# Kernel tuning notes

Measured on AMD Instinct MI355X. Metric: run time of the kernel, lower is better.

The kernel has to match this reference:

```python
import jax, jax.numpy as jnp
import numpy as np

D_MODEL = 768
N_HEADS = 12
N_KV = 4
D_HEAD = 64
WINDOW = 512
GLOBAL = 64
THETA = 10000.0


def setup_inputs() -> dict:
    key = jax.random.key(0)
    ks = jax.random.split(key, 5)
    B, T = 2, 2048
    s = D_MODEL ** -0.5
    return {
        "x": jax.random.normal(ks[0], (B, T, D_MODEL), jnp.float32),
        "wq": jax.random.normal(ks[1], (D_MODEL, N_HEADS * D_HEAD), jnp.float32) * s,
        "wk": jax.random.normal(ks[2], (D_MODEL, N_KV * D_HEAD), jnp.float32) * s,
        "wv": jax.random.normal(ks[3], (D_MODEL, N_KV * D_HEAD), jnp.float32) * s,
        "wo": jax.random.normal(ks[4], (N_HEADS * D_HEAD, D_MODEL), jnp.float32) * s,
    }


def _rotate_half(x):
    h = x.shape[-1] // 2
    return jnp.concatenate([-x[..., h:], x[..., :h]], axis=-1)


def _rope_tables(T, dtype):
    inv_freq = 1.0 / (THETA ** (jnp.arange(0, D_HEAD, 2, dtype=jnp.float32) / D_HEAD))
    freqs = jnp.outer(jnp.arange(T, dtype=jnp.float32), inv_freq)  # [T, D_HEAD/2]
    emb = jnp.concatenate([freqs, freqs], axis=-1)  # [T, D_HEAD]
    return jnp.cos(emb).astype(dtype), jnp.sin(emb).astype(dtype)


def reference(x, wq, wk, wv, wo):
    B, T, _ = x.shape
    # projections -> [B, H, T, D]
    q = (x @ wq).reshape(B, T, N_HEADS, D_HEAD).transpose(0, 2, 1, 3)
    k = (x @ wk).reshape(B, T, N_KV, D_HEAD).transpose(0, 2, 1, 3)
    v = (x @ wv).reshape(B, T, N_KV, D_HEAD).transpose(0, 2, 1, 3)
    # RoPE (broadcast [T,D] over batch/heads)
    cos, sin = _rope_tables(T, x.dtype)
    q = q * cos + _rotate_half(q) * sin
    k = k * cos + _rotate_half(k) * sin
    new_k, new_v = k, v  # kv cache before GQA expansion
    # GQA expansion: each kv head repeated kv_groups consecutive times
    groups = N_HEADS // N_KV
    k = jnp.repeat(k, groups, axis=1)
    v = jnp.repeat(v, groups, axis=1)
    scale = jnp.asarray(D_HEAD, x.dtype) ** 0.5
    scores = jnp.einsum("bhqd,bhkd->bhqk", q, k) / scale
    # sliding-window causal + global-token mask (Longformer-style)
    i = jnp.arange(T)[:, None]
    j = jnp.arange(T)[None, :]
    allowed = (j <= i) & ((j > i - WINDOW) | (j < GLOBAL) | (i < GLOBAL))
    scores = jnp.where(allowed, scores, -jnp.inf)
    weights = jax.nn.softmax(scores, axis=-1)
    out = jnp.einsum("bhqk,bhkd->bhqd", weights, v)
    out = out.transpose(0, 2, 1, 3).reshape(B, T, N_HEADS * D_HEAD)
    return out @ wo, (new_k, new_v)
```

## Files before the change

### kernel.cpp

```cpp
#include <hip/hip_runtime.h>
#include <hip/hip_bf16.h>

#define BATCH 2
#define SEQ 2048
#define DMODEL 768
#define NHEADS 12
#define NKV 4
#define DHEAD 64
#define WIN 512
#define GLB 64
#define ROWS (BATCH * SEQ)

typedef short short8 __attribute__((ext_vector_type(8)));
typedef float f32x4 __attribute__((ext_vector_type(4)));

__device__ inline short f2bs(float f) {
    unsigned u = __float_as_uint(f);
    return (short)((u + 0x7fffu + ((u >> 16) & 1u)) >> 16);
}

__device__ inline void cp16(const short* g, short* l) {
    __builtin_amdgcn_global_load_lds(
        (const __attribute__((address_space(1))) unsigned int*)g,
        (__attribute__((address_space(3))) unsigned int*)l, 16, 0, 0);
}

__global__ __launch_bounds__(256) void transp_all(
    const float* __restrict__ wq, const float* __restrict__ wk,
    const float* __restrict__ wv, const float* __restrict__ wo,
    short* __restrict__ wqkvT, short* __restrict__ woT,
    const float* __restrict__ x, short* __restrict__ xb) {
    __shared__ float t[32][33];
    int bid = blockIdx.x;
    if (bid >= 1536) {
        const long i = ((long)(bid - 1536) * 256 + threadIdx.x) * 8;
        float ff[8];
        *(float4*)&ff[0] = ((const float4*)(x + i))[0];
        *(float4*)&ff[4] = ((const float4*)(x + i))[1];
        short8 o;
#pragma unroll
        for (int j = 0; j < 8; ++j) o[j] = f2bs(ff[j]);
        *(short8*)(xb + i) = o;
        return;
    }
    const float* src; short* dst; int N;
    if (bid < 576)      { src = wq; dst = wqkvT; N = DMODEL; }
    else if (bid < 768) { src = wk; dst = wqkvT + DMODEL * DMODEL; N = 256; bid -= 576; }
    else if (bid < 960) { src = wv; dst = wqkvT + (DMODEL + 256) * DMODEL; N = 256; bid -= 768; }
    else                { src = wo; dst = woT; N = DMODEL; bid -= 960; }
    const int ntx = N >> 5;
    const int k0 = (bid / ntx) << 5, n0 = (bid % ntx) << 5;
    const int x_ = threadIdx.x & 31, y = threadIdx.x >> 5;
#pragma unroll
    for (int i = 0; i < 32; i += 8)
        t[y + i][x_] = src[(long)(k0 + y + i) * N + n0 + x_];
    __syncthreads();
#pragma unroll
    for (int i = 0; i < 32; i += 8)
        dst[(long)(n0 + y + i) * DMODEL + k0 + x_] = f2bs(t[x_][y + i]);
}

template <int MODE>
__global__ __launch_bounds__(256) void gemm_tn(
    const short* __restrict__ A, const short* __restrict__ Bt,
    float* __restrict__ Cq, float* __restrict__ Ck, float* __restrict__ Cv,
    short* __restrict__ Kb, short* __restrict__ Vt, int M, int N, int K) {
    __shared__ short As_[2][64 * 64];
    __shared__ short Bs_[2][128 * 64];
    const int tid = threadIdx.x;
    const int lane = tid & 63, w = tid >> 6;
    const int m_ = lane & 15, quad = lane >> 4;
    const int sw = m_ & 7;
    const int wm = w >> 1, wn = w & 1;
    const long bm = (long)blockIdx.y * 64, bn = (long)blockIdx.x * 128;
    const int soff = (lane >> 3) * K + (((lane & 7) ^ (lane >> 3)) << 3);

    f32x4 acc[2][4];
#pragma unroll
    for (int i = 0; i < 2; ++i)
#pragma unroll
        for (int j = 0; j < 4; ++j) acc[i][j] = (f32x4){0.f, 0.f, 0.f, 0.f};

    auto stage = [&](int k0, int bs) {
#pragma unroll
        for (int r = 0; r < 6; ++r) {
            const int ch = w * 6 + r;
            if (ch < 8)
                cp16(A + (bm + (ch << 3)) * K + k0 + soff, &As_[bs][ch << 9]);
            else
                cp16(Bt + (bn + ((ch - 8) << 3)) * K + k0 + soff,
                     &Bs_[bs][(ch - 8) << 9]);
        }
    };

    stage(0, 0);
    asm volatile("s_waitcnt vmcnt(0)" ::: "memory");
    asm volatile("s_barrier" ::: "memory");

    const int nk = K >> 6;
    for (int ks = 0; ks < nk; ++ks) {
        const int bs = ks & 1;
        if (ks + 1 < nk) stage((ks + 1) << 6, bs ^ 1);
#pragma unroll
        for (int kh = 0; kh < 2; ++kh) {
            short8 af[2], bf[4];
#pragma unroll
            for (int i = 0; i < 2; ++i)
                af[i] = *(const short8*)&As_[bs][(wm * 32 + i * 16 + m_) * 64 + (((kh * 4 + quad) ^ sw) << 3)];
#pragma unroll
            for (int j = 0; j < 4; ++j)
                bf[j] = *(const short8*)&Bs_[bs][(wn * 64 + j * 16 + m_) * 64 + (((kh * 4 + quad) ^ sw) << 3)];
            __builtin_amdgcn_s_setprio(1);
#pragma unroll
            for (int i = 0; i < 2; ++i)
#pragma unroll
                for (int j = 0; j < 4; ++j)
                    acc[i][j] = __builtin_amdgcn_mfma_f32_16x16x32_bf16(af[i], bf[j], acc[i][j], 0, 0, 0);
            __builtin_amdgcn_s_setprio(0);
        }
        if (ks + 1 < nk) {
            asm volatile("s_waitcnt vmcnt(0)" ::: "memory");
            asm volatile("s_barrier" ::: "memory");
        }
    }

    if (MODE == 0 || bn < DMODEL) {
        const int stride = (MODE == 1) ? DMODEL : N;
#pragma unroll
        for (int i = 0; i < 2; ++i) {
            const int row0 = (int)bm + wm * 32 + i * 16 + quad * 4;
#pragma unroll
            for (int j = 0; j < 4; ++j) {
                const int col = (int)bn + wn * 64 + j * 16 + m_;
#pragma unroll
                for (int r = 0; r < 4; ++r)
                    Cq[(long)(row0 + r) * stride + col] = acc[i][j][r];
            }
        }
    } else if (bn < DMODEL + 256) {
        const int kvh = ((int)(bn - DMODEL) >> 6) + wn;
#pragma unroll
        for (int i = 0; i < 2; ++i) {
            const int row0 = (int)bm + wm * 32 + i * 16 + quad * 4;
            const int t = row0 & (SEQ - 1), b = row0 >> 11;
            const long base0 = ((long)(b * NKV + kvh) * SEQ) << 6;
#pragma unroll
            for (int j = 0; j < 2; ++j) {
                const int d = j * 16 + m_;
                const float invf = expf(-(float)d * 0.2878231366f);
#pragma unroll
                for (int r = 0; r < 4; ++r) {
                    const int tt = t + r;
                    float s_, c_;
                    sincosf((float)tt * invf, &s_, &c_);
                    const float x1 = acc[i][j][r], x2 = acc[i][j + 2][r];
                    const float y1 = x1 * c_ - x2 * s_;
                    const float y2 = x2 * c_ + x1 * s_;
                    const long o = base0 + ((long)tt << 6) + d;
                    Ck[o] = y1;
                    Ck[o + 32] = y2;
                    Kb[o] = f2bs(y1);
                    Kb[o + 32] = f2bs(y2);
                }
            }
        }
    } else {
        const int kvh = ((int)(bn - (DMODEL + 256)) >> 6) + wn;
#pragma unroll
        for (int i = 0; i < 2; ++i) {
            const int row0 = (int)bm + wm * 32 + i * 16 + quad * 4;
            const int t = row0 & (SEQ - 1), b = row0 >> 11;
            const long bkvi = (long)(b * NKV + kvh);
            const long vtbase = (bkvi << 17) + ((long)(t >> 6) << 12) + (t & 63);
#pragma unroll
            for (int j = 0; j < 4; ++j) {
                const int d = j * 16 + m_;
                union { short sh[4]; unsigned long long u; } pk;
#pragma unroll
                for (int r = 0; r < 4; ++r) {
                    const float v = acc[i][j][r];
                    Cv[((bkvi * SEQ + t + r) << 6) + d] = v;
                    pk.sh[r] = f2bs(v);
                }
                *(unsigned long long*)&Vt[vtbase + ((long)d << 6)] = pk.u;
            }
        }
    }
}

__global__ __launch_bounds__(384) void flash6(
    const float* __restrict__ Qf, const short* __restrict__ Kb,
    const short* __restrict__ Vt, short* __restrict__ ATT) {
    __shared__ short Kbuf[2][64 * 64];
    __shared__ short Vbuf[2][64 * 64];
    __shared__ short Pl[6][16 * 64];
    const int tid = threadIdx.x;
    const int w = tid >> 6, lane = tid & 63;
    const int m_ = lane & 15, quad = lane >> 4;
    const int sw = m_ & 7;
    const int bkv = blockIdx.x >> 6;
    const int t0 = (63 - (blockIdx.x & 63)) << 5;
    const int b = bkv >> 2, kvh = bkv & 3;
    const int h = kvh * 3 + (w >> 1);
    const int qg = w & 1;
    const int trw = t0 + (qg << 4);
    const int tq = trw + m_;
    const long kgb = ((long)bkv * SEQ) << 6;
    const long vgb = (long)bkv * SEQ * DHEAD;

    const int soff = ((lane >> 3) << 6) + (((lane & 7) ^ (lane >> 3)) << 3);

    short8 qf0, qf1;
    {
        const float* qpf = Qf + (long)(b * SEQ + tq) * DMODEL + h * DHEAD + quad * 8;
        float xx[8], yy[8];
        *(float4*)&xx[0] = ((const float4*)qpf)[0];
        *(float4*)&xx[4] = ((const float4*)qpf)[1];
        *(float4*)&yy[0] = ((const float4*)(qpf + 32))[0];
        *(float4*)&yy[4] = ((const float4*)(qpf + 32))[1];
#pragma unroll
        for (int jj = 0; jj < 8; ++jj) {
            const int j = quad * 8 + jj;
            const float inv = expf(-(float)j * 0.2878231366f);
            float s_, c_;
            sincosf((float)tq * inv, &s_, &c_);
            qf0[jj] = f2bs((xx[jj] * c_ - yy[jj] * s_) * 0.125f);
            qf1[jj] = f2bs((yy[jj] * c_ + xx[jj] * s_) * 0.125f);
        }
    }

    f32x4 of[4];
#pragma unroll
    for (int i = 0; i < 4; ++i) of[i] = (f32x4){0.f, 0.f, 0.f, 0.f};
    float mr = -1e30f, lr = 0.f;

    int wlo = t0 - (WIN - 1);
    if (wlo < GLB) wlo = GLB;
    wlo &= ~63;
    const int nwin = (t0 + 31 >= wlo) ? (((t0 + 31 - wlo) >> 6) + 1) : 0;
    const int ntile = 1 + nwin;
    auto kb_of = [&](int j) { return (j == 0) ? 0 : (wlo + ((j - 1) << 6)); };

    auto stage = [&](int kb, int bs) {
#pragma unroll
        for (int r = 0; r < 3; ++r) {
            const int ch = w + 6 * r;
            if (ch < 8) {
                cp16(Kb + kgb + ((long)(kb + (ch << 3)) << 6) + soff,
                     &Kbuf[bs][ch << 9]);
            } else if (ch < 16) {
                const int cv = ch - 8;
                cp16(Vt + vgb + (((long)kb >> 6) << 12) + (cv << 9) + soff,
                     &Vbuf[bs][cv << 9]);
            }
        }
    };

    stage(kb_of(0), 0);
    asm volatile("s_waitcnt vmcnt(0)" ::: "memory");
    asm volatile("s_barrier" ::: "memory");

    for (int tI = 0; tI < ntile; ++tI) {
        const int kb = kb_of(tI);
        const int bs = tI & 1;
        if (tI + 1 < ntile) stage(kb_of(tI + 1), bs ^ 1);

        short8 kf[8], vf[8];
#pragma unroll
        for (int st = 0; st < 4; ++st)
#pragma unroll
            for (int hh = 0; hh < 2; ++hh)
                kf[st * 2 + hh] = *(const short8*)&Kbuf[bs][(st * 16 + m_) * 64 + (((hh * 4 + quad) ^ sw) << 3)];
#pragma unroll
        for (int dt = 0; dt < 4; ++dt)
#pragma unroll
            for (int kh = 0; kh < 2; ++kh)
                vf[dt * 2 + kh] = *(const short8*)&Vbuf[bs][(dt * 16 + m_) * 64 + (((kh * 4 + quad) ^ sw) << 3)];

        f32x4 s[4];
        __builtin_amdgcn_s_setprio(1);
#pragma unroll
        for (int st = 0; st < 4; ++st) {
            f32x4 a = (f32x4){0.f, 0.f, 0.f, 0.f};
            a = __builtin_amdgcn_mfma_f32_16x16x32_bf16(kf[st * 2 + 0], qf0, a, 0, 0, 0);
            a = __builtin_amdgcn_mfma_f32_16x16x32_bf16(kf[st * 2 + 1], qf1, a, 0, 0, 0);
            s[st] = a;
        }
        __builtin_amdgcn_s_setprio(0);

        const bool fully = (kb + 63 <= trw) &&
                           ((kb >= trw + 16 - WIN) || (kb + 63 < GLB) || (trw + 15 < GLB));
        if (!fully) {
#pragma unroll
            for (int st = 0; st < 4; ++st) {
#pragma unroll
                for (int r = 0; r < 4; ++r) {
                    const int key = kb + st * 16 + quad * 4 + r;
                    const bool ok = (key <= tq) && ((key > tq - WIN) || (key < GLB) || (tq < GLB));
                    if (!ok) s[st][r] = -1e30f;
                }
            }
        }

        float tm = -1e30f;
#pragma unroll
        for (int st = 0; st < 4; ++st)
#pragma unroll
            for (int r = 0; r < 4; ++r) tm = fmaxf(tm, s[st][r]);
        tm = fmaxf(tm, __shfl_xor(tm, 16, 64));
        tm = fmaxf(tm, __shfl_xor(tm, 32, 64));
        if (!__all(tm <= mr)) {
            const float mnew = fmaxf(mr, tm);
            const float alpha = __expf(mr - mnew);
            mr = mnew;
            lr *= alpha;
#pragma unroll
            for (int dt = 0; dt < 4; ++dt)
#pragma unroll
                for (int r = 0; r < 4; ++r) of[dt][r] *= alpha;
        }
        float rs = 0.f;
#pragma unroll
        for (int st = 0; st < 4; ++st) {
            float p0 = __expf(s[st][0] - mr);
            float p1 = __expf(s[st][1] - mr);
            float p2 = __expf(s[st][2] - mr);
            float p3 = __expf(s[st][3] - mr);
            rs += (p0 + p1) + (p2 + p3);
            union { short sh[4]; unsigned long long u; } pk;
            pk.sh[0] = f2bs(p0); pk.sh[1] = f2bs(p1);
            pk.sh[2] = f2bs(p2); pk.sh[3] = f2bs(p3);
            *(unsigned long long*)&Pl[w][m_ * 64 + (((st * 2 + (quad >> 1)) ^ sw) << 3) + ((quad & 1) << 2)] = pk.u;
        }
        rs += __shfl_xor(rs, 16, 64);
        rs += __shfl_xor(rs, 32, 64);
        lr += rs;

        short8 pf[2];
#pragma unroll
        for (int kh = 0; kh < 2; ++kh)
            pf[kh] = *(const short8*)&Pl[w][m_ * 64 + (((kh * 4 + quad) ^ sw) << 3)];

        __builtin_amdgcn_s_setprio(1);
#pragma unroll
        for (int dt = 0; dt < 4; ++dt) {
            of[dt] = __builtin_amdgcn_mfma_f32_16x16x32_bf16(vf[dt * 2 + 0], pf[0], of[dt], 0, 0, 0);
            of[dt] = __builtin_amdgcn_mfma_f32_16x16x32_bf16(vf[dt * 2 + 1], pf[1], of[dt], 0, 0, 0);
        }
        __builtin_amdgcn_s_setprio(0);

        if (tI + 1 < ntile) {
            asm volatile("s_waitcnt vmcnt(0)" ::: "memory");
            asm volatile("s_barrier" ::: "memory");
        }
    }

    const float inv = 1.0f / lr;
    short* op = ATT + (long)(b * SEQ + tq) * DMODEL + h * DHEAD + quad * 4;
#pragma unroll
    for (int dt = 0; dt < 4; ++dt) {
        union { short sh[4]; unsigned long long u; } pk;
#pragma unroll
        for (int r = 0; r < 4; ++r) pk.sh[r] = f2bs(of[dt][r] * inv);
        *(unsigned long long*)(op + dt * 16) = pk.u;
    }
}

extern "C" void kernel_launch(void* const* d_in, const int* in_sizes, int n_in,
                              void* d_out, int out_size, void* d_ws, size_t ws_size,
                              hipStream_t stream) {
    const float* x = (const float*)d_in[0];
    const float* wq = (const float*)d_in[1];
    const float* wk = (const float*)d_in[2];
    const float* wv = (const float*)d_in[3];
    const float* wo = (const float*)d_in[4];
    float* out = (float*)d_out;
    float* out_k = out + (long)ROWS * DMODEL;
    float* out_v = out_k + (long)BATCH * NKV * SEQ * DHEAD;

    short* regA = (short*)d_ws;
    short* wqkvT = regA;
    short* ATTb = regA;
    short* woT = regA + (long)ROWS * DMODEL;
    short* KbB = woT + (long)DMODEL * DMODEL;
    short* VtB = KbB + (long)BATCH * NKV * SEQ * DHEAD;
    short* xb = VtB + (long)BATCH * NKV * SEQ * DHEAD;

    transp_all<<<3072, 256, 0, stream>>>(wq, wk, wv, wo, wqkvT, woT, x, xb);
    gemm_tn<1><<<dim3((DMODEL + 2 * NKV * DHEAD) / 128, ROWS / 64), 256, 0, stream>>>(
        xb, wqkvT, out, out_k, out_v, KbB, VtB, ROWS, DMODEL + 2 * NKV * DHEAD, DMODEL);
    flash6<<<BATCH * NKV * (SEQ / 32), 384, 0, stream>>>(out, KbB, VtB, ATTb);
    gemm_tn<0><<<dim3(DMODEL / 128, ROWS / 64), 256, 0, stream>>>(
        ATTb, woT, out, nullptr, nullptr, nullptr, nullptr, ROWS, DMODEL, DMODEL);
}
```

Before: 134.7 us.

## Triple-buffer LDS tiles with prefetch distance two in GEMM and flash kernels

Both the projection GEMM and the sliding-window flash-attention kernel move from double to triple LDS buffering. Tiles are now prefetched two iterations ahead, and partial s_waitcnt vmcnt counts replace full drains so that one load stays in flight during compute. The flash kernel's staging is reworked so that four of its six waves each issue four loads, which gives a uniform vmcnt count. The aim is to hide more global-load latency, at the cost of more LDS per block, which may lower occupancy.

```diff
diff --git a/kernel.cpp b/kernel.cpp
--- a/kernel.cpp
+++ b/kernel.cpp
@@ -65,8 +65,8 @@
     const short* __restrict__ A, const short* __restrict__ Bt,
     float* __restrict__ Cq, float* __restrict__ Ck, float* __restrict__ Cv,
     short* __restrict__ Kb, short* __restrict__ Vt, int M, int N, int K) {
-    __shared__ short As_[2][64 * 64];
-    __shared__ short Bs_[2][128 * 64];
+    __shared__ short As_[3][64 * 64];
+    __shared__ short Bs_[3][128 * 64];
     const int tid = threadIdx.x;
     const int lane = tid & 63, w = tid >> 6;
     const int m_ = lane & 15, quad = lane >> 4;
@@ -93,14 +93,15 @@
         }
     };
 
+    const int nk = K >> 6;
     stage(0, 0);
-    asm volatile("s_waitcnt vmcnt(0)" ::: "memory");
+    stage(64, 1);
+    asm volatile("s_waitcnt vmcnt(6)" ::: "memory");
     asm volatile("s_barrier" ::: "memory");
 
-    const int nk = K >> 6;
     for (int ks = 0; ks < nk; ++ks) {
-        const int bs = ks & 1;
-        if (ks + 1 < nk) stage((ks + 1) << 6, bs ^ 1);
+        const int bs = ks % 3;
+        if (ks + 2 < nk) stage((ks + 2) << 6, (ks + 2) % 3);
 #pragma unroll
         for (int kh = 0; kh < 2; ++kh) {
             short8 af[2], bf[4];
@@ -119,7 +120,10 @@
             __builtin_amdgcn_s_setprio(0);
         }
         if (ks + 1 < nk) {
-            asm volatile("s_waitcnt vmcnt(0)" ::: "memory");
+            if (ks + 2 < nk)
+                asm volatile("s_waitcnt vmcnt(6)" ::: "memory");
+            else
+                asm volatile("s_waitcnt vmcnt(0)" ::: "memory");
             asm volatile("s_barrier" ::: "memory");
         }
     }
@@ -191,8 +195,8 @@
 __global__ __launch_bounds__(384) void flash6(
     const float* __restrict__ Qf, const short* __restrict__ Kb,
     const short* __restrict__ Vt, short* __restrict__ ATT) {
-    __shared__ short Kbuf[2][64 * 64];
-    __shared__ short Vbuf[2][64 * 64];
+    __shared__ short Kbuf[3][64 * 64];
+    __shared__ short Vbuf[3][64 * 64];
     __shared__ short Pl[6][16 * 64];
     const int tid = threadIdx.x;
     const int w = tid >> 6, lane = tid & 63;
@@ -242,28 +246,33 @@
     auto kb_of = [&](int j) { return (j == 0) ? 0 : (wlo + ((j - 1) << 6)); };
 
     auto stage = [&](int kb, int bs) {
-#pragma unroll
-        for (int r = 0; r < 3; ++r) {
-            const int ch = w + 6 * r;
-            if (ch < 8) {
-                cp16(Kb + kgb + ((long)(kb + (ch << 3)) << 6) + soff,
-                     &Kbuf[bs][ch << 9]);
-            } else if (ch < 16) {
-                const int cv = ch - 8;
-                cp16(Vt + vgb + (((long)kb >> 6) << 12) + (cv << 9) + soff,
-                     &Vbuf[bs][cv << 9]);
+        if (w < 4) {
+#pragma unroll
+            for (int r = 0; r < 4; ++r) {
+                const int ch = (w << 2) | r;
+                if (ch < 8)
+                    cp16(Kb + kgb + ((long)(kb + (ch << 3)) << 6) + soff,
+                         &Kbuf[bs][ch << 9]);
+                else
+                    cp16(Vt + vgb + (((long)kb >> 6) << 12) + ((ch - 8) << 9) + soff,
+                         &Vbuf[bs][(ch - 8) << 9]);
             }
         }
     };
 
     stage(kb_of(0), 0);
-    asm volatile("s_waitcnt vmcnt(0)" ::: "memory");
+    if (ntile > 1) {
+        stage(kb_of(1), 1);
+        asm volatile("s_waitcnt vmcnt(4)" ::: "memory");
+    } else {
+        asm volatile("s_waitcnt vmcnt(0)" ::: "memory");
+    }
     asm volatile("s_barrier" ::: "memory");
 
     for (int tI = 0; tI < ntile; ++tI) {
         const int kb = kb_of(tI);
-        const int bs = tI & 1;
-        if (tI + 1 < ntile) stage(kb_of(tI + 1), bs ^ 1);
+        const int bs = tI % 3;
+        if (tI + 2 < ntile) stage(kb_of(tI + 2), (tI + 2) % 3);
 
         short8 kf[8], vf[8];
 #pragma unroll
@@ -350,7 +359,10 @@
         __builtin_amdgcn_s_setprio(0);
 
         if (tI + 1 < ntile) {
-            asm volatile("s_waitcnt vmcnt(0)" ::: "memory");
+            if (tI + 2 < ntile)
+                asm volatile("s_waitcnt vmcnt(4)" ::: "memory");
+            else
+                asm volatile("s_waitcnt vmcnt(0)" ::: "memory");
             asm volatile("s_barrier" ::: "memory");
         }
     }
```

Result: slower. 144.3 us (+7.1%).
